# Performance work log

Hardware: AMD Instinct MI355X
Metric: run time of the kernel (lower is better)

The kernel has to match this reference:

```python
import jax, jax.numpy as jnp
import numpy as np

B, T, D, H = 4, 4096, 2048, 128  # head_size = embedding_size // num_heads = 2048 // 16

def setup_inputs() -> dict:
    key = jax.random.key(0)
    kx, kq, kk, kv = jax.random.split(key, 4)
    x = jax.random.normal(kx, (B, T, D), dtype=jnp.float32)
    # Dense kernels with normal(0.01) init as in the module
    Wq = 0.01 * jax.random.normal(kq, (D, H), dtype=jnp.float32)
    Wk = 0.01 * jax.random.normal(kk, (D, H), dtype=jnp.float32)
    Wv = 0.01 * jax.random.normal(kv, (D, H), dtype=jnp.float32)
    return {"x": x, "Wq": Wq, "Wk": Wk, "Wv": Wv}

def reference(x, Wq, Wk, Wv):
    # Q/K/V projections: Dense(features=head_size, use_bias=False)
    Q = jnp.einsum('BTD,DH->BTH', x, Wq)
    K = jnp.einsum('BTD,DH->BTH', x, Wk)
    V = jnp.einsum('BTD,DH->BTH', x, Wv)
    scale = 1.0 / jnp.sqrt(jnp.asarray(K.shape[-1], dtype=x.dtype))
    scores = jnp.einsum('BTH,BSH->BTS', Q, K) * scale  # (B, T, T)
    weights = jax.nn.softmax(scores, axis=-1)
    # dropout rate 0.0 (deterministic) -> identity
    out = jnp.einsum('BTS,BSH->BTH', weights, V)  # (B, T, H)
    return out
```

## Files before the change

kernel.cpp:

```cpp
#include <hip/hip_runtime.h>
#include <hip/hip_bf16.h>
#include <math.h>

#define B_ 4
#define T_ 4096
#define D_ 2048
#define H_ 128
#define M_ (B_*T_)

typedef __bf16 bf16;
typedef __attribute__((ext_vector_type(8))) __bf16 bf16x8;
typedef __attribute__((ext_vector_type(4))) float f32x4;

#define MFMA(a,b,c) __builtin_amdgcn_mfma_f32_16x16x32_bf16(a,b,c,0,0,0)

typedef __attribute__((address_space(3))) unsigned int lds_u32_t;
typedef const __attribute__((address_space(1))) unsigned int glb_u32_t;

__device__ __forceinline__ void cp16(void* lds, const void* g) {
    __builtin_amdgcn_global_load_lds((glb_u32_t*)g, (lds_u32_t*)lds, 16, 0, 0);
}

#define QOFF   0u
#define KOFF   (4u<<20)
#define VTOFF  (8u<<20)
#define WTOFF  (12u<<20)
#define OPOFF  (14u<<20)
#define LPOFF  (OPOFF + 8388608u)

__global__ __launch_bounds__(256) void cvtw_kernel(
    const float* __restrict__ Wq, const float* __restrict__ Wk,
    const float* __restrict__ Wv, bf16* __restrict__ Wtb)
{
    int id = blockIdx.x * 256 + threadIdx.x;
    int mat = id >> 15;
    int rem = id & 32767;
    int n = rem >> 8, kc = rem & 255;
    const float* W = (mat == 0) ? Wq : ((mat == 1) ? Wk : Wv);
    bf16x8 v;
    #pragma unroll
    for (int j = 0; j < 8; j++)
        v[j] = (bf16)W[(size_t)(kc*8 + j) * H_ + n];
    *(bf16x8*)((char*)Wtb + (size_t)mat*524288 + (size_t)n*4096 + kc*16) = v;
}

__global__ __launch_bounds__(256) void proj_kernel(
    const float* __restrict__ X, const bf16* __restrict__ Wtb,
    bf16* __restrict__ Qb, bf16* __restrict__ Kb, bf16* __restrict__ Vtb)
{
    __shared__ __align__(16) char smem[58368];
    char* xs = smem;
    char* Ws = smem + 9216;

    const int tid = threadIdx.x;
    const int w = tid >> 6, lane = tid & 63;
    const int c = lane & 15, quad = lane >> 4;
    const int m0 = blockIdx.x * 64;

    f32x4 acc[3][8];
    #pragma unroll
    for (int m = 0; m < 3; m++)
        #pragma unroll
        for (int ct = 0; ct < 8; ct++) acc[m][ct] = (f32x4){0.f,0.f,0.f,0.f};

    for (int it = 0; it < 32; it++) {
        const int k0 = it * 64;
        __syncthreads();
        #pragma unroll
        for (int u = 0; u < 4; u++) {
            int id = tid + u*256;
            int r = id >> 4, f4 = id & 15;
            float4 v = *(const float4*)(X + (size_t)(m0 + r)*D_ + k0 + f4*4);
            union { bf16 h[4]; uint2 u2; } pk;
            pk.h[0] = (bf16)v.x; pk.h[1] = (bf16)v.y;
            pk.h[2] = (bf16)v.z; pk.h[3] = (bf16)v.w;
            *(uint2*)(xs + r*144 + f4*8) = pk.u2;
        }
        #pragma unroll
        for (int mat = 0; mat < 3; mat++) {
            #pragma unroll
            for (int u = 0; u < 4; u++) {
                int s = tid + u*256;
                int n = s >> 3, ccsw = s & 7;
                int cc = (ccsw ^ n) & 7;
                const char* src = (const char*)Wtb + (size_t)mat*524288
                                + (size_t)n*4096 + k0*2 + cc*16;
                cp16(Ws + mat*16384 + s*16, src);
            }
        }
        __syncthreads();

        bf16x8 af[2];
        #pragma unroll
        for (int kk = 0; kk < 2; kk++)
            af[kk] = *(const bf16x8*)(xs + (w*16 + c)*144 + quad*16 + kk*64);
        #pragma unroll
        for (int mat = 0; mat < 3; mat++) {
            #pragma unroll
            for (int ct = 0; ct < 8; ct++) {
                int n = ct*16 + c;
                #pragma unroll
                for (int kk = 0; kk < 2; kk++) {
                    int cc = quad + 4*kk;
                    int slot = n*8 + ((cc ^ n) & 7);
                    bf16x8 bfg = *(const bf16x8*)(Ws + mat*16384 + slot*16);
                    acc[mat][ct] = MFMA(af[kk], bfg, acc[mat][ct]);
                }
            }
        }
    }

    const float qscale = 0.08838834764831845f;
    bf16* outg0 = Qb; bf16* outg1 = Kb;
    #pragma unroll
    for (int mat = 0; mat < 2; mat++) {
        __syncthreads();
        bf16* U = (bf16*)smem;
        #pragma unroll
        for (int ct = 0; ct < 8; ct++)
            #pragma unroll
            for (int r = 0; r < 4; r++) {
                float v = acc[mat][ct][r];
                if (mat == 0) v *= qscale;
                U[(w*16 + quad*4 + r)*136 + ct*16 + c] = (bf16)v;
            }
        __syncthreads();
        bf16* og = (mat == 0) ? outg0 : outg1;
        #pragma unroll
        for (int u = 0; u < 4; u++) {
            int id = tid + u*256;
            int r = id >> 4, cc = id & 15;
            bf16x8 vv = *(const bf16x8*)(smem + r*272 + cc*16);
            *(bf16x8*)((char*)og + (size_t)(m0 + r)*256 + cc*16) = vv;
        }
    }
    #pragma unroll
    for (int ct = 0; ct < 8; ct++) {
        int n = ct*16 + c;
        int m = m0 + w*16 + quad*4;
        union { bf16 h[4]; uint2 u2; } pk;
        #pragma unroll
        for (int r = 0; r < 4; r++) pk.h[r] = (bf16)acc[2][ct][r];
        *(uint2*)((char*)Vtb + (size_t)n*32768 + (size_t)m*2) = pk.u2;
    }
}

__global__ __launch_bounds__(256) void attn_kernel(
    const bf16* __restrict__ Qb, const bf16* __restrict__ Kb,
    const bf16* __restrict__ Vtb,
    float* __restrict__ Out0, float* __restrict__ Opart1,
    float* __restrict__ lpart)
{
    __shared__ __align__(16) char Ks[16384];
    __shared__ __align__(16) char Vs[16384];
    __shared__ __align__(16) char Ps[9216];

    const int tid = threadIdx.x;
    const int w = tid >> 6, lane = tid & 63;
    const int c = lane & 15, quad = lane >> 4;

    const int bx = blockIdx.x;
    const int qt = bx & 63;
    const int b  = (bx >> 6) & 3;
    const int ks = bx >> 8;
    const int row0 = b*T_ + qt*64;

    bf16x8 qf[4];
    {
        const char* qrow = (const char*)Qb + (size_t)(row0 + w*16 + c)*256 + quad*16;
        #pragma unroll
        for (int kk = 0; kk < 4; kk++)
            qf[kk] = *(const bf16x8*)(qrow + kk*64);
    }

    f32x4 o[8];
    #pragma unroll
    for (int i = 0; i < 8; i++) o[i] = (f32x4){0.f,0.f,0.f,0.f};
    float lsum[4] = {0.f, 0.f, 0.f, 0.f};

    for (int it = 0; it < 32; it++) {
        const int k0 = ks*2048 + it*64;
        __syncthreads();
        #pragma unroll
        for (int u = 0; u < 4; u++) {
            int s = tid + u*256;
            int r = s >> 4, csw = s & 15;
            int cg = (csw & 8) | ((csw ^ r) & 7);
            const char* src = (const char*)Kb + (size_t)(b*T_ + k0 + r)*256 + cg*16;
            cp16(Ks + s*16, src);
        }
        #pragma unroll
        for (int u = 0; u < 4; u++) {
            int s = tid + u*256;
            int h = s >> 3, ccsw = s & 7;
            int cc = (ccsw ^ h) & 7;
            const char* src = (const char*)Vtb + (size_t)h*32768
                            + (size_t)(b*T_ + k0)*2 + cc*16;
            cp16(Vs + s*16, src);
        }
        __syncthreads();

        #pragma unroll
        for (int ct = 0; ct < 4; ct++) {
            f32x4 s4 = (f32x4){0.f,0.f,0.f,0.f};
            int row = ct*16 + c;
            #pragma unroll
            for (int kk = 0; kk < 4; kk++) {
                int cg = quad + 4*kk;
                int slot = row*16 + (((cg ^ row) & 7) | (cg & 8));
                bf16x8 kf = *(const bf16x8*)(Ks + slot*16);
                s4 = MFMA(qf[kk], kf, s4);
            }
            #pragma unroll
            for (int r = 0; r < 4; r++) {
                float p = __expf(s4[r]);
                lsum[r] += p;
                ((bf16*)Ps)[(w*16 + quad*4 + r)*72 + ct*16 + c] = (bf16)p;
            }
        }
        #pragma unroll
        for (int kk = 0; kk < 2; kk++) {
            bf16x8 pf = *(const bf16x8*)(Ps + (w*16 + c)*144 + quad*16 + kk*64);
            #pragma unroll
            for (int ct = 0; ct < 8; ct++) {
                int n = ct*16 + c;
                int cc = quad + 4*kk;
                int slot = n*8 + ((cc ^ n) & 7);
                bf16x8 vf = *(const bf16x8*)(Vs + slot*16);
                o[ct] = MFMA(pf, vf, o[ct]);
            }
        }
    }

    #pragma unroll
    for (int r = 0; r < 4; r++) {
        float v = lsum[r];
        #pragma unroll
        for (int off = 1; off < 16; off <<= 1)
            v += __shfl_xor(v, off, 64);
        if (c == 0)
            lpart[ks*M_ + row0 + w*16 + quad*4 + r] = v;
    }
    float* Od = (ks == 0) ? Out0 : Opart1;
    #pragma unroll
    for (int ct = 0; ct < 8; ct++)
        #pragma unroll
        for (int r = 0; r < 4; r++)
            Od[(size_t)(row0 + w*16 + quad*4 + r)*H_ + ct*16 + c] = o[ct][r];
}

__global__ __launch_bounds__(256) void merge_kernel(
    float* __restrict__ Out, const float* __restrict__ Op1,
    const float* __restrict__ lp)
{
    int id = blockIdx.x * 256 + threadIdx.x;
    int row = id >> 5;
    float inv = 1.0f / (lp[row] + lp[M_ + row]);
    float4 a = *(const float4*)(Out + (size_t)id*4);
    float4 bq = *(const float4*)(Op1 + (size_t)id*4);
    float4 rr;
    rr.x = (a.x + bq.x) * inv; rr.y = (a.y + bq.y) * inv;
    rr.z = (a.z + bq.z) * inv; rr.w = (a.w + bq.w) * inv;
    *(float4*)(Out + (size_t)id*4) = rr;
}

extern "C" void kernel_launch(void* const* d_in, const int* in_sizes, int n_in,
                              void* d_out, int out_size, void* d_ws, size_t ws_size,
                              hipStream_t stream) {
    const float* x  = (const float*)d_in[0];
    const float* Wq = (const float*)d_in[1];
    const float* Wk = (const float*)d_in[2];
    const float* Wv = (const float*)d_in[3];
    float* outp = (float*)d_out;
    char* ws = (char*)d_ws;

    bf16* Qb  = (bf16*)(ws + QOFF);
    bf16* Kb  = (bf16*)(ws + KOFF);
    bf16* Vtb = (bf16*)(ws + VTOFF);
    bf16* Wtb = (bf16*)(ws + WTOFF);
    float* Op1 = (float*)(ws + OPOFF);
    float* lp  = (float*)(ws + LPOFF);

    cvtw_kernel<<<384, 256, 0, stream>>>(Wq, Wk, Wv, Wtb);
    proj_kernel<<<M_/64, 256, 0, stream>>>(x, Wtb, Qb, Kb, Vtb);
    attn_kernel<<<512, 256, 0, stream>>>(Qb, Kb, Vtb, outp, Op1, lp);
    merge_kernel<<<2048, 256, 0, stream>>>(outp, Op1, lp);
}
```

Measured before the change: 324.9 us.

## Double-buffer projection GEMM with 32x32 MFMA and coalesced weight transpose

Rewrites the QKV projection kernel to double-buffer the X and weight tiles in LDS, so the next k-slice's global loads are issued while the current slice is multiplied. Each wave now computes a 64x96 tile with 32x32x16 MFMAs instead of 16x16x32 ones, which gives more reuse per LDS fragment read. The weight-conversion kernel now transposes through shared memory with coalesced reads and folds the Q scale into Wq. The cost is 112KB of LDS with launch_bounds(256,1), so only one block fits per CU and occupancy is limited.

```diff
diff --git a/kernel.cpp b/kernel.cpp
--- a/kernel.cpp
+++ b/kernel.cpp
@@ -11,8 +11,10 @@
 typedef __bf16 bf16;
 typedef __attribute__((ext_vector_type(8))) __bf16 bf16x8;
 typedef __attribute__((ext_vector_type(4))) float f32x4;
-
-#define MFMA(a,b,c) __builtin_amdgcn_mfma_f32_16x16x32_bf16(a,b,c,0,0,0)
+typedef __attribute__((ext_vector_type(16))) float f32x16;
+
+#define MFMA16(a,b,c) __builtin_amdgcn_mfma_f32_16x16x32_bf16(a,b,c,0,0,0)
+#define MFMA32(a,b,c) __builtin_amdgcn_mfma_f32_32x32x16_bf16(a,b,c,0,0,0)
 
 typedef __attribute__((address_space(3))) unsigned int lds_u32_t;
 typedef const __attribute__((address_space(1))) unsigned int glb_u32_t;
@@ -32,116 +34,197 @@
     const float* __restrict__ Wq, const float* __restrict__ Wk,
     const float* __restrict__ Wv, bf16* __restrict__ Wtb)
 {
-    int id = blockIdx.x * 256 + threadIdx.x;
-    int mat = id >> 15;
-    int rem = id & 32767;
-    int n = rem >> 8, kc = rem & 255;
-    const float* W = (mat == 0) ? Wq : ((mat == 1) ? Wk : Wv);
-    bf16x8 v;
-    #pragma unroll
-    for (int j = 0; j < 8; j++)
-        v[j] = (bf16)W[(size_t)(kc*8 + j) * H_ + n];
-    *(bf16x8*)((char*)Wtb + (size_t)mat*524288 + (size_t)n*4096 + kc*16) = v;
-}
-
-__global__ __launch_bounds__(256) void proj_kernel(
+    __shared__ __align__(16) bf16 U[128 * 72];
+    const int tid = threadIdx.x;
+    const int m  = blockIdx.x >> 5;
+    const int kt = blockIdx.x & 31;
+    const int k0 = kt * 64;
+    const float* W = (m == 0) ? Wq : ((m == 1) ? Wk : Wv);
+    const float sc = (m == 0) ? 0.08838834764831845f : 1.0f;
+
+    #pragma unroll
+    for (int u = 0; u < 8; u++) {
+        int id = tid + u * 256;
+        int kr = id >> 5, c4 = id & 31;
+        float4 v = *(const float4*)(W + (size_t)(k0 + kr) * H_ + c4 * 4);
+        U[(c4*4 + 0) * 72 + kr] = (bf16)(v.x * sc);
+        U[(c4*4 + 1) * 72 + kr] = (bf16)(v.y * sc);
+        U[(c4*4 + 2) * 72 + kr] = (bf16)(v.z * sc);
+        U[(c4*4 + 3) * 72 + kr] = (bf16)(v.w * sc);
+    }
+    __syncthreads();
+    #pragma unroll
+    for (int u = 0; u < 4; u++) {
+        int id = tid + u * 256;
+        int n = id >> 3, kc = id & 7;
+        bf16x8 v = *(const bf16x8*)((const char*)U + n * 144 + kc * 16);
+        *(bf16x8*)((char*)Wtb + (size_t)m * 524288 + (size_t)n * 4096
+                   + k0 * 2 + kc * 16) = v;
+    }
+}
+
+__global__ __launch_bounds__(256, 1) void proj_kernel(
     const float* __restrict__ X, const bf16* __restrict__ Wtb,
     bf16* __restrict__ Qb, bf16* __restrict__ Kb, bf16* __restrict__ Vtb)
 {
-    __shared__ __align__(16) char smem[58368];
-    char* xs = smem;
-    char* Ws = smem + 9216;
+    __shared__ __align__(16) char smem[114688];
 
     const int tid = threadIdx.x;
-    const int w = tid >> 6, lane = tid & 63;
-    const int c = lane & 15, quad = lane >> 4;
+    const int lane = tid & 63;
+    const int ng = tid >> 6;
+    const int c31 = lane & 31;
+    const int kh = lane >> 5;
     const int m0 = blockIdx.x * 64;
 
-    f32x4 acc[3][8];
-    #pragma unroll
-    for (int m = 0; m < 3; m++)
-        #pragma unroll
-        for (int ct = 0; ct < 8; ct++) acc[m][ct] = (f32x4){0.f,0.f,0.f,0.f};
+    f32x16 acc[2][3];
+    #pragma unroll
+    for (int mt = 0; mt < 2; mt++)
+        #pragma unroll
+        for (int t = 0; t < 3; t++)
+            #pragma unroll
+            for (int r = 0; r < 16; r++) acc[mt][t][r] = 0.f;
+
+
+    {
+        char* w0 = smem + 16384;
+        #pragma unroll
+        for (int u = 0; u < 12; u++) {
+            int s = tid + u * 256;
+            int n = s >> 3, ccs = s & 7;
+            int kc = ccs ^ (n & 7);
+            int mat = n >> 7, ncol = n & 127;
+            cp16(w0 + s * 16,
+                 (const char*)Wtb + (size_t)mat * 524288 + (size_t)ncol * 4096 + kc * 16);
+        }
+        #pragma unroll
+        for (int u = 0; u < 2; u++) {
+            int id = tid + u * 256;
+            int r = id >> 3, cc = id & 7;
+            const float* src = X + (size_t)(m0 + r) * D_ + cc * 8;
+            float4 v0 = *(const float4*)src;
+            float4 v1 = *(const float4*)(src + 4);
+            union { bf16 h[8]; uint4 u4; } pk;
+            pk.h[0]=(bf16)v0.x; pk.h[1]=(bf16)v0.y; pk.h[2]=(bf16)v0.z; pk.h[3]=(bf16)v0.w;
+            pk.h[4]=(bf16)v1.x; pk.h[5]=(bf16)v1.y; pk.h[6]=(bf16)v1.z; pk.h[7]=(bf16)v1.w;
+            int slot = r * 8 + (cc ^ (r & 7));
+            *(uint4*)(smem + slot * 16) = pk.u4;
+        }
+    }
+    __syncthreads();
 
     for (int it = 0; it < 32; it++) {
-        const int k0 = it * 64;
-        __syncthreads();
+        const int cur = it & 1, nxt = cur ^ 1;
+        const int k1 = (it + 1) * 64;
+        char* xcur = smem + cur * 8192;
+        char* xnxt = smem + nxt * 8192;
+        char* wcur = smem + 16384 + cur * 49152;
+        char* wnxt = smem + 16384 + nxt * 49152;
+        float4 xv[4];
+        if (it < 31) {
+            #pragma unroll
+            for (int u = 0; u < 12; u++) {
+                int s = tid + u * 256;
+                int n = s >> 3, ccs = s & 7;
+                int kc = ccs ^ (n & 7);
+                int mat = n >> 7, ncol = n & 127;
+                cp16(wnxt + s * 16,
+                     (const char*)Wtb + (size_t)mat * 524288 + (size_t)ncol * 4096
+                     + k1 * 2 + kc * 16);
+            }
+            #pragma unroll
+            for (int u = 0; u < 2; u++) {
+                int id = tid + u * 256;
+                int r = id >> 3, cc = id & 7;
+                const float* src = X + (size_t)(m0 + r) * D_ + k1 + cc * 8;
+                xv[u*2+0] = *(const float4*)src;
+                xv[u*2+1] = *(const float4*)(src + 4);
+            }
+        }
+        #pragma unroll
+        for (int ks = 0; ks < 4; ks++) {
+            const int kc = ks * 2 + kh;
+            bf16x8 a[2], bq[3];
+            #pragma unroll
+            for (int mt = 0; mt < 2; mt++) {
+                int r = mt * 32 + c31;
+                int slot = r * 8 + (kc ^ (r & 7));
+                a[mt] = *(const bf16x8*)(xcur + slot * 16);
+            }
+            #pragma unroll
+            for (int t = 0; t < 3; t++) {
+                int n = ng * 96 + t * 32 + c31;
+                int slot = n * 8 + (kc ^ (n & 7));
+                bq[t] = *(const bf16x8*)(wcur + slot * 16);
+            }
+            #pragma unroll
+            for (int mt = 0; mt < 2; mt++)
+                #pragma unroll
+                for (int t = 0; t < 3; t++)
+                    acc[mt][t] = MFMA32(a[mt], bq[t], acc[mt][t]);
+        }
+        if (it < 31) {
+            #pragma unroll
+            for (int u = 0; u < 2; u++) {
+                int id = tid + u * 256;
+                int r = id >> 3, cc = id & 7;
+                union { bf16 h[8]; uint4 u4; } pk;
+                float4 v0 = xv[u*2+0], v1 = xv[u*2+1];
+                pk.h[0]=(bf16)v0.x; pk.h[1]=(bf16)v0.y; pk.h[2]=(bf16)v0.z; pk.h[3]=(bf16)v0.w;
+                pk.h[4]=(bf16)v1.x; pk.h[5]=(bf16)v1.y; pk.h[6]=(bf16)v1.z; pk.h[7]=(bf16)v1.w;
+                int slot = r * 8 + (cc ^ (r & 7));
+                *(uint4*)(xnxt + slot * 16) = pk.u4;
+            }
+        }
+        __syncthreads();
+    }
+
+    #pragma unroll
+    for (int mt = 0; mt < 2; mt++) {
+        #pragma unroll
+        for (int t = 0; t < 3; t++) {
+            int nb = ng * 96 + t * 32;
+            if ((nb >> 7) == 2) {
+                int ncol = (nb & 127) + c31;
+                #pragma unroll
+                for (int g = 0; g < 4; g++) {
+                    int m = m0 + mt * 32 + g * 8 + kh * 4;
+                    union { bf16 h[4]; uint2 u2; } pk;
+                    #pragma unroll
+                    for (int e = 0; e < 4; e++)
+                        pk.h[e] = (bf16)acc[mt][t][g*4 + e];
+                    *(uint2*)((char*)Vtb + (size_t)ncol * 32768 + (size_t)m * 2) = pk.u2;
+                }
+            }
+        }
+    }
+    bf16* U = (bf16*)smem;
+    #pragma unroll
+    for (int mat = 0; mat < 2; mat++) {
+        __syncthreads();
+        #pragma unroll
+        for (int mt = 0; mt < 2; mt++) {
+            #pragma unroll
+            for (int t = 0; t < 3; t++) {
+                int nb = ng * 96 + t * 32;
+                if ((nb >> 7) == mat) {
+                    int lcol = (nb & 127) + c31;
+                    #pragma unroll
+                    for (int r = 0; r < 16; r++) {
+                        int row = (r & 3) + 8 * (r >> 2) + 4 * kh;
+                        U[(mt*32 + row) * 136 + lcol] = (bf16)acc[mt][t][r];
+                    }
+                }
+            }
+        }
+        __syncthreads();
+        bf16* og = (mat == 0) ? Qb : Kb;
         #pragma unroll
         for (int u = 0; u < 4; u++) {
-            int id = tid + u*256;
-            int r = id >> 4, f4 = id & 15;
-            float4 v = *(const float4*)(X + (size_t)(m0 + r)*D_ + k0 + f4*4);
-            union { bf16 h[4]; uint2 u2; } pk;
-            pk.h[0] = (bf16)v.x; pk.h[1] = (bf16)v.y;
-            pk.h[2] = (bf16)v.z; pk.h[3] = (bf16)v.w;
-            *(uint2*)(xs + r*144 + f4*8) = pk.u2;
-        }
-        #pragma unroll
-        for (int mat = 0; mat < 3; mat++) {
-            #pragma unroll
-            for (int u = 0; u < 4; u++) {
-                int s = tid + u*256;
-                int n = s >> 3, ccsw = s & 7;
-                int cc = (ccsw ^ n) & 7;
-                const char* src = (const char*)Wtb + (size_t)mat*524288
-                                + (size_t)n*4096 + k0*2 + cc*16;
-                cp16(Ws + mat*16384 + s*16, src);
-            }
-        }
-        __syncthreads();
-
-        bf16x8 af[2];
-        #pragma unroll
-        for (int kk = 0; kk < 2; kk++)
-            af[kk] = *(const bf16x8*)(xs + (w*16 + c)*144 + quad*16 + kk*64);
-        #pragma unroll
-        for (int mat = 0; mat < 3; mat++) {
-            #pragma unroll
-            for (int ct = 0; ct < 8; ct++) {
-                int n = ct*16 + c;
-                #pragma unroll
-                for (int kk = 0; kk < 2; kk++) {
-                    int cc = quad + 4*kk;
-                    int slot = n*8 + ((cc ^ n) & 7);
-                    bf16x8 bfg = *(const bf16x8*)(Ws + mat*16384 + slot*16);
-                    acc[mat][ct] = MFMA(af[kk], bfg, acc[mat][ct]);
-                }
-            }
-        }
-    }
-
-    const float qscale = 0.08838834764831845f;
-    bf16* outg0 = Qb; bf16* outg1 = Kb;
-    #pragma unroll
-    for (int mat = 0; mat < 2; mat++) {
-        __syncthreads();
-        bf16* U = (bf16*)smem;
-        #pragma unroll
-        for (int ct = 0; ct < 8; ct++)
-            #pragma unroll
-            for (int r = 0; r < 4; r++) {
-                float v = acc[mat][ct][r];
-                if (mat == 0) v *= qscale;
-                U[(w*16 + quad*4 + r)*136 + ct*16 + c] = (bf16)v;
-            }
-        __syncthreads();
-        bf16* og = (mat == 0) ? outg0 : outg1;
-        #pragma unroll
-        for (int u = 0; u < 4; u++) {
-            int id = tid + u*256;
-            int r = id >> 4, cc = id & 15;
-            bf16x8 vv = *(const bf16x8*)(smem + r*272 + cc*16);
-            *(bf16x8*)((char*)og + (size_t)(m0 + r)*256 + cc*16) = vv;
-        }
-    }
-    #pragma unroll
-    for (int ct = 0; ct < 8; ct++) {
-        int n = ct*16 + c;
-        int m = m0 + w*16 + quad*4;
-        union { bf16 h[4]; uint2 u2; } pk;
-        #pragma unroll
-        for (int r = 0; r < 4; r++) pk.h[r] = (bf16)acc[2][ct][r];
-        *(uint2*)((char*)Vtb + (size_t)n*32768 + (size_t)m*2) = pk.u2;
+            int id = tid + u * 256;
+            int rr = id >> 4, cc = id & 15;
+            bf16x8 v = *(const bf16x8*)((const char*)U + rr * 272 + cc * 16);
+            *(bf16x8*)((char*)og + (size_t)(m0 + rr) * 256 + cc * 16) = v;
+        }
     }
 }
 
@@ -209,7 +292,7 @@
                 int cg = quad + 4*kk;
                 int slot = row*16 + (((cg ^ row) & 7) | (cg & 8));
                 bf16x8 kf = *(const bf16x8*)(Ks + slot*16);
-                s4 = MFMA(qf[kk], kf, s4);
+                s4 = MFMA16(qf[kk], kf, s4);
             }
             #pragma unroll
             for (int r = 0; r < 4; r++) {
@@ -227,7 +310,7 @@
                 int cc = quad + 4*kk;
                 int slot = n*8 + ((cc ^ n) & 7);
                 bf16x8 vf = *(const bf16x8*)(Vs + slot*16);
-                o[ct] = MFMA(pf, vf, o[ct]);
+                o[ct] = MFMA16(pf, vf, o[ct]);
             }
         }
     }
@@ -281,7 +364,7 @@
     float* Op1 = (float*)(ws + OPOFF);
     float* lp  = (float*)(ws + LPOFF);
 
-    cvtw_kernel<<<384, 256, 0, stream>>>(Wq, Wk, Wv, Wtb);
+    cvtw_kernel<<<96, 256, 0, stream>>>(Wq, Wk, Wv, Wtb);
     proj_kernel<<<M_/64, 256, 0, stream>>>(x, Wtb, Qb, Kb, Vtb);
     attn_kernel<<<512, 256, 0, stream>>>(Qb, Kb, Vtb, outp, Op1, lp);
     merge_kernel<<<2048, 256, 0, stream>>>(outp, Op1, lp);
```

Result: faster. 291.3 us (-10.3%).
